# Optimization experiments

Measured on AMD Instinct MI355X. Metric: run time of the kernel, lower is better.

## Reference

```python
import jax, jax.numpy as jnp
import numpy as np

B, S, H, D = 4, 1024, 16, 64
DIM = H * D          # 1024
FF_INNER = 4 * DIM   # 4096
ROT_BASE = 1000.0


def _l2norm(x):
    # F.normalize(p=2, dim=-1): x / max(||x||_2, 1e-12)
    n = jnp.linalg.norm(x, axis=-1, keepdims=True)
    return x / jnp.maximum(n, 1e-12)


def _rmsnorm(x):
    return x * jax.lax.rsqrt(jnp.mean(x * x, axis=-1, keepdims=True) + jnp.finfo(jnp.float32).eps)


def _rope_tables(seq, d, base):
    inv_freq = base ** (-(jnp.arange(0, d, 2, dtype=jnp.float32) / d))
    freqs = jnp.outer(jnp.arange(seq, dtype=jnp.float32), inv_freq)  # [S, D/2]
    # original caches cos/sin in bfloat16
    cos = jnp.cos(freqs).astype(jnp.bfloat16)[None, :, None, :]
    sin = jnp.sin(freqs).astype(jnp.bfloat16)[None, :, None, :]
    return cos, sin


def _rope(x, cos, sin):
    d = x.shape[3] // 2
    x1, x2 = x[..., :d], x[..., d:]
    y1 = x1 * cos + x2 * sin
    y2 = -x1 * sin + x2 * cos
    return jnp.concatenate([y1, y2], axis=3).astype(x.dtype)


def setup_inputs() -> dict:
    key = jax.random.key(0)
    ks = jax.random.split(key, 12)
    w = lambda k, shp: 0.02 * jax.random.normal(k, shp, dtype=jnp.float32)
    inp = {
        'h_states': jax.random.normal(ks[0], (B, S, DIM), dtype=jnp.float32),
        'attention_mask': jnp.tril(jnp.ones((S, S), dtype=jnp.float32))[None].repeat(B, axis=0),
        'Wq': w(ks[1], (DIM, DIM)), 'Wk': w(ks[2], (DIM, DIM)), 'Wv': w(ks[3], (DIM, DIM)),
        'WqB': w(ks[4], (DIM, DIM)), 'WkB': w(ks[5], (DIM, DIM)),
        'Wo': w(ks[6], (DIM, DIM)), 'bo': jnp.zeros((DIM,), jnp.float32),
        'Wff_in': w(ks[7], (DIM, 2 * FF_INNER)), 'bff_in': jnp.zeros((2 * FF_INNER,), jnp.float32),
        'Wff_out': w(ks[8], (FF_INNER, DIM)), 'bff_out': jnp.zeros((DIM,), jnp.float32),
        'learnedlambda': jnp.asarray(1.0, jnp.float32),
        'l2normscale': jnp.log(jnp.asarray(float(S) ** 2 - float(S), jnp.float32)),
    }
    return inp


def reference(h_states, attention_mask, Wq, Wk, Wv, WqB, WkB, Wo, bo,
              Wff_in, bff_in, Wff_out, bff_out, learnedlambda, l2normscale):
    inner = _rmsnorm(h_states)                               # layerwisenorm (rmsnorm, no affine)
    scale = D ** -0.5

    def proj(Wm):
        return (inner @ Wm).reshape(B, S, H, D)
    q, k, v = proj(Wq), proj(Wk), proj(Wv)
    bq, bk = proj(WqB), proj(WkB)

    cos, sin = _rope_tables(S, D, ROT_BASE)
    q = _rope(_l2norm(q), cos, sin)
    k = _rope(_l2norm(k), cos, sin)
    bq = _rope(_l2norm(bq), cos, sin)
    bk = _rope(_l2norm(bk), cos, sin)

    # main branch: causal softmax attention, scale=1, scaled by learned l2normscale
    scores = jnp.einsum('bihd,bjhd->bhij', q, k)             # [B,H,S,S]
    causal = jnp.tril(jnp.ones((S, S), dtype=bool))
    scores = jnp.where(causal, scores, -jnp.inf)
    attn = jax.nn.softmax(scores, axis=-1)
    y = l2normscale * jnp.einsum('bhij,bjhd->bihd', attn, v)  # [B,S,H,D]

    # bias branch: softmax-free masked scores @ ones == row-sum broadcast over D
    bscores = jnp.einsum('bihd,bjhd->bhij', bq, bk) * scale
    bscores = bscores * attention_mask[:, None, :, :]
    brow = bscores.sum(axis=-1)                               # [B,H,S]
    y = y + jnp.transpose(brow, (0, 2, 1))[..., None]         # broadcast over D

    attn_out = y.reshape(B, S, DIM) @ Wo + bo

    # SwiGLU FFN: chunk -> x, gate; silu(gate) * x
    u = inner @ Wff_in + bff_in
    xh, gate = jnp.split(u, 2, axis=-1)
    dense_out = (jax.nn.silu(gate) * xh) @ Wff_out + bff_out

    return h_states * learnedlambda + dense_out + attn_out
```

## Files before the change

kernel.cpp:

```cpp
#include <hip/hip_runtime.h>
#include <stdint.h>
#include <math.h>

typedef float f32x4 __attribute__((ext_vector_type(4)));
typedef short s16x8 __attribute__((ext_vector_type(8)));
typedef unsigned short bfu;

#define AS1q const __attribute__((address_space(1))) void*
#define AS3q __attribute__((address_space(3))) void*

static __device__ __forceinline__ float bf2f(bfu v) {
  return __uint_as_float(((unsigned int)v) << 16);
}
static __device__ __forceinline__ bfu f2bf(float f) {
  unsigned int u = __float_as_uint(f);
  return (bfu)((u + 0x7fffu + ((u >> 16) & 1u)) >> 16);
}

struct PreArgs {
  const float* w5[5];
  const float* Wffin;
  const float* Wffout;
  const float* Wo;
  const float* h;
  bfu* wt5; bfu* wtfi; bfu* wtfoc;
  bfu* cosb; bfu* sinb; bfu* inner;
};
__global__ __launch_bounds__(256) void prologue_k(PreArgs a) {
  __shared__ float shmem[32 * 33];
  int id = blockIdx.x;
  if (id < 18432) {
    const float* W; bfu* Wt; int K, N, dstride, dofs, mode, nb, kb;
    if (id < 5120) {
      int z = id >> 10, rem = id & 1023;
      W = a.w5[z]; Wt = a.wt5 + ((size_t)z << 20);
      K = 1024; N = 1024; dstride = 1024; dofs = 0; mode = 0;
      nb = (rem & 31) << 5; kb = (rem >> 5) << 5;
    } else if (id < 13312) {
      int id2 = id - 5120;
      W = a.Wffin; Wt = a.wtfi; K = 1024; N = 8192; dstride = 1024; dofs = 0; mode = 1;
      nb = (id2 & 255) << 5; kb = (id2 >> 8) << 5;
    } else if (id < 17408) {
      int id3 = id - 13312;
      W = a.Wffout; Wt = a.wtfoc; K = 4096; N = 1024; dstride = 5120; dofs = 0; mode = 2;
      nb = (id3 & 31) << 5; kb = (id3 >> 5) << 5;
    } else {
      int id4 = id - 17408;
      W = a.Wo; Wt = a.wtfoc; K = 1024; N = 1024; dstride = 5120; dofs = 4096; mode = 2;
      nb = (id4 & 31) << 5; kb = (id4 >> 5) << 5;
    }
    float (*t)[33] = reinterpret_cast<float(*)[33]>(shmem);
    int tx = threadIdx.x & 31, ty = threadIdx.x >> 5;
#pragma unroll
    for (int i = 0; i < 4; i++) {
      int r = ty + i * 8;
      t[r][tx] = W[(size_t)(kb + r) * N + nb + tx];
    }
    __syncthreads();
#pragma unroll
    for (int i = 0; i < 4; i++) {
      int r = ty + i * 8;
      int n = nb + r;
      int nd = n;
      if (mode == 1) { int j = n & 4095, isg = n >> 12; nd = ((j >> 4) << 5) | (isg << 4) | (j & 15); }
      int k = kb + tx;
      int kp = (mode == 2) ? (((k >> 5) << 5) | ((k & 15) << 1) | ((k >> 4) & 1)) : k;
      Wt[(size_t)nd * dstride + dofs + kp] = f2bf(t[tx][r]);
    }
  } else if (id < 18560) {
    int idx = (id - 18432) * 256 + threadIdx.x;
    int s = idx >> 5, i = idx & 31;
    float f = powf(1000.0f, -(float)i / 32.0f);
    float fr = (float)s * f;
    a.cosb[idx] = f2bf(cosf(fr));
    a.sinb[idx] = f2bf(sinf(fr));
  } else {
    int row = id - 18560;
    const float* hr = a.h + (size_t)row * 1024;
    f32x4 x = *reinterpret_cast<const f32x4*>(hr + threadIdx.x * 4);
    float ss = x[0] * x[0] + x[1] * x[1] + x[2] * x[2] + x[3] * x[3];
    for (int off = 32; off; off >>= 1) ss += __shfl_down(ss, off);
    int wave = threadIdx.x >> 6, lane = threadIdx.x & 63;
    if (lane == 0) shmem[wave] = ss;
    __syncthreads();
    float tot = shmem[0] + shmem[1] + shmem[2] + shmem[3];
    float r = rsqrtf(tot * (1.0f / 1024.0f) + 1.1920929e-07f);
    bfu* o = a.inner + (size_t)row * 1024 + threadIdx.x * 4;
    o[0] = f2bf(x[0] * r); o[1] = f2bf(x[1] * r);
    o[2] = f2bf(x[2] * r); o[3] = f2bf(x[3] * r);
  }
}

__global__ __launch_bounds__(512, 2) void fused_k(const bfu* __restrict__ q, const bfu* __restrict__ k,
                                                  const bfu* __restrict__ vT,
                                                  const float* __restrict__ brow,
                                                  const float* __restrict__ l2p,
                                                  const bfu* __restrict__ A, const bfu* __restrict__ Bt,
                                                  bfu* __restrict__ AB,
                                                  const float* __restrict__ bias) {
  __shared__ __align__(16) char lds[131072];
  int tid = threadIdx.x, w = tid >> 6, lane = tid & 63;
  int g = lane >> 4, l15 = lane & 15;

  if (blockIdx.x < 256) {
    int fid = blockIdx.x + ((w >> 2) << 8);
    int sub = fid & 255;
    int qt = (fid >> 8) ? 7 - (sub >> 6) : (sub >> 6);
    int bh = sub & 63;
    const size_t bhofs = (size_t)bh << 16;
    int rt0 = qt * 128 + (w & 3) * 32;
    bfu* P = reinterpret_cast<bfu*>(lds) + (size_t)w * (2 * 16 * 72);

    s16x8 aq[2][2];
#pragma unroll
    for (int m = 0; m < 2; m++)
#pragma unroll
      for (int ks = 0; ks < 2; ks++)
        aq[m][ks] = *reinterpret_cast<const s16x8*>(
            q + bhofs + (size_t)(rt0 + m * 16 + l15) * 64 + ks * 32 + g * 8);

    f32x4 O[2][4];
    float mr[2][4], lr[2][4];
#pragma unroll
    for (int m = 0; m < 2; m++)
#pragma unroll
      for (int r = 0; r < 4; r++) { O[m][r] = (f32x4){0.f, 0.f, 0.f, 0.f}; mr[m][r] = -3.0e38f; lr[m][r] = 0.f; }

    s16x8 kA[4][2], kB[4][2];
    auto loadK = [&](s16x8 (&kd)[4][2], int jt) {
#pragma unroll
      for (int nt = 0; nt < 4; nt++)
#pragma unroll
        for (int ks = 0; ks < 2; ks++)
          kd[nt][ks] = *reinterpret_cast<const s16x8*>(
              k + bhofs + (size_t)(jt * 64 + nt * 16 + l15) * 64 + ks * 32 + g * 8);
    };

    int njt = 2 * qt + 2;
    loadK(kA, 0);

    auto body = [&](int jt, s16x8 (&kc)[4][2], s16x8 (&kn)[4][2], bool pf) {
      s16x8 vv[4][2];
#pragma unroll
      for (int nt = 0; nt < 4; nt++)
#pragma unroll
        for (int ks = 0; ks < 2; ks++)
          vv[nt][ks] = *reinterpret_cast<const s16x8*>(
              vT + ((size_t)(bh * 64 + nt * 16 + l15) << 10) + jt * 64 + ks * 32 + g * 8);

      bool act[2] = { jt * 64 <= rt0 + 15, jt * 64 <= rt0 + 31 };
      f32x4 sfr[2][4];
#pragma unroll
      for (int m = 0; m < 2; m++) {
        if (!act[m]) continue;
#pragma unroll
        for (int nt = 0; nt < 4; nt++) {
          sfr[m][nt] = (f32x4){0.f, 0.f, 0.f, 0.f};
#pragma unroll
          for (int ks = 0; ks < 2; ks++)
            sfr[m][nt] = __builtin_amdgcn_mfma_f32_16x16x32_bf16(aq[m][ks], kc[nt][ks], sfr[m][nt], 0, 0, 0);
        }
      }
      if (pf) loadK(kn, jt + 1);

#pragma unroll
      for (int m = 0; m < 2; m++) {
        if (!act[m]) continue;
        int rtm = rt0 + m * 16;
        if (jt * 64 + 63 > rtm) {
#pragma unroll
          for (int ntn = 0; ntn < 4; ntn++)
#pragma unroll
            for (int r = 0; r < 4; r++)
              if (jt * 64 + ntn * 16 + l15 > rtm + g * 4 + r) sfr[m][ntn][r] = -1e30f;
        }
        float alpha[4];
#pragma unroll
        for (int r = 0; r < 4; r++) {
          float v = fmaxf(fmaxf(sfr[m][0][r], sfr[m][1][r]), fmaxf(sfr[m][2][r], sfr[m][3][r]));
#pragma unroll
          for (int m2 = 1; m2 < 16; m2 <<= 1) v = fmaxf(v, __shfl_xor(v, m2));
          float mn = fmaxf(mr[m][r], v);
          alpha[r] = __expf(mr[m][r] - mn);
          mr[m][r] = mn;
        }
#pragma unroll
        for (int r = 0; r < 4; r++) {
          float rs = 0.f;
#pragma unroll
          for (int ntn = 0; ntn < 4; ntn++) {
            float e = __expf(sfr[m][ntn][r] - mr[m][r]);
            rs += e;
            P[(m * 16 + g * 4 + r) * 72 + ntn * 16 + l15] = f2bf(e);
          }
#pragma unroll
          for (int m2 = 1; m2 < 16; m2 <<= 1) rs += __shfl_xor(rs, m2);
          lr[m][r] = lr[m][r] * alpha[r] + rs;
#pragma unroll
          for (int ntn = 0; ntn < 4; ntn++) O[m][ntn][r] *= alpha[r];
        }
      }
      asm volatile("s_waitcnt lgkmcnt(0)" ::: "memory");
      __builtin_amdgcn_sched_barrier(0);
#pragma unroll
      for (int m = 0; m < 2; m++) {
        if (!act[m]) continue;
        s16x8 pa[2];
#pragma unroll
        for (int ks = 0; ks < 2; ks++)
          pa[ks] = *reinterpret_cast<const s16x8*>(&P[(m * 16 + l15) * 72 + ks * 32 + g * 8]);
#pragma unroll
        for (int nt = 0; nt < 4; nt++)
#pragma unroll
          for (int ks = 0; ks < 2; ks++)
            O[m][nt] = __builtin_amdgcn_mfma_f32_16x16x32_bf16(pa[ks], vv[nt][ks], O[m][nt], 0, 0, 0);
      }
    };

    for (int jt = 0; jt < njt; jt += 2) {
      body(jt, kA, kB, true);
      body(jt + 1, kB, kA, jt + 2 < njt);
    }

    float l2ns = l2p[0];
    int b = bh >> 4, hq = bh & 15;
#pragma unroll
    for (int m = 0; m < 2; m++)
#pragma unroll
      for (int r = 0; r < 4; r++) {
        int rowg = rt0 + m * 16 + g * 4 + r;
        float br = brow[bh * 1024 + rowg];
        float sc = l2ns / lr[m][r];
        float v0 = O[m][0][r] * sc + br;
        float v1 = O[m][1][r] * sc + br;
        float v2 = O[m][2][r] * sc + br;
        float v3 = O[m][3][r] * sc + br;
        unsigned int p01 = (unsigned int)f2bf(v0) | ((unsigned int)f2bf(v1) << 16);
        unsigned int p23 = (unsigned int)f2bf(v2) | ((unsigned int)f2bf(v3) << 16);
        size_t base = (size_t)(b * 1024 + rowg) * 5120 + 4096 + hq * 64;
        *reinterpret_cast<unsigned int*>(AB + base + 2 * l15) = p01;
        *reinterpret_cast<unsigned int*>(AB + base + 32 + 2 * l15) = p23;
      }
    return;
  }

  int id0 = blockIdx.x - 256;
  int c = id0 & 7, rr = id0 >> 3;
  int bn0 = (c & 3) * 8, bm0 = (c >> 2) * 8;
  int bm = bm0 + rr / 8, bn = bn0 + rr % 8;
  int wm = w >> 2, wn = w & 3;
  const int K = 1024;
  const int NT = 16, NI = 8;

  f32x4 acc[8][4];
#pragma unroll
  for (int m = 0; m < 8; m++)
#pragma unroll
    for (int n = 0; n < 4; n++) acc[m][n] = (f32x4){0.f, 0.f, 0.f, 0.f};

  s16x8 af[4][2];
  s16x8 bfr[4][2];

  auto stage = [&](int mat, int kt, int hf) {
    if (kt >= NT) return;
    int d = kt & 1;
    const bfu* s0 = (mat == 0) ? A : Bt;
    int rowbase = ((mat == 0) ? bm : bn) * 256 + hf * 128;
    int k0 = kt << 6;
    char* base = lds + d * 65536 + mat * 32768 + hf * 16384;
#pragma unroll
    for (int r = 0; r < 2; r++) {
      int L = r * 512 + tid;
      int row = L >> 3, cc = L & 7;
      int kc = cc ^ (row & 7);
      const bfu* src = s0 + (size_t)(rowbase + row) * K + k0 + kc * 8;
      char* dst = base + r * 8192 + w * 1024;
      __builtin_amdgcn_global_load_lds((AS1q)src, (AS3q)dst, 16, 0, 0);
    }
  };

  auto ldA = [&](int d, int mh) {
    const char* base = lds + d * 65536 + wm * 16384;
#pragma unroll
    for (int mm = 0; mm < 4; mm++) {
      int row = mh * 64 + mm * 16 + l15;
#pragma unroll
      for (int ks = 0; ks < 2; ks++)
        af[mm][ks] = *reinterpret_cast<const s16x8*>(
            base + row * 128 + (((ks * 4 + g) ^ (row & 7)) << 4));
    }
  };
  auto ldB2 = [&](int d, int nh) {
    const char* base = lds + d * 65536 + 32768 + (wn >> 1) * 16384;
#pragma unroll
    for (int nn = 0; nn < 2; nn++) {
      int row = (wn & 1) * 64 + (nh * 2 + nn) * 16 + l15;
#pragma unroll
      for (int ks = 0; ks < 2; ks++)
        bfr[nh * 2 + nn][ks] = *reinterpret_cast<const s16x8*>(
            base + row * 128 + (((ks * 4 + g) ^ (row & 7)) << 4));
    }
  };
  auto mfma_q = [&](int mh, int nh) {
    asm volatile("s_waitcnt lgkmcnt(0)" ::: "memory");
    __builtin_amdgcn_sched_barrier(0);
    __builtin_amdgcn_s_barrier();
    __builtin_amdgcn_s_setprio(1);
#pragma unroll
    for (int mm = 0; mm < 4; mm++)
#pragma unroll
      for (int nn = 0; nn < 2; nn++) {
        int n = nh * 2 + nn, m = mh * 4 + mm;
#pragma unroll
        for (int ks = 0; ks < 2; ks++)
          acc[m][n] = __builtin_amdgcn_mfma_f32_16x16x32_bf16(af[mm][ks], bfr[n][ks], acc[m][n], 0, 0, 0);
      }
    __builtin_amdgcn_s_setprio(0);
    __builtin_amdgcn_sched_barrier(0);
  };

  stage(1, 0, 0); stage(0, 0, 0); stage(0, 0, 1); stage(1, 0, 1);
  stage(1, 1, 0); stage(1, 1, 1);
  asm volatile("s_waitcnt vmcnt(4)" ::: "memory");
  __builtin_amdgcn_s_barrier();
  __builtin_amdgcn_sched_barrier(0);

  for (int i = 0; i < NI; i++) {
    int t0 = 2 * i, t1 = 2 * i + 1;
    bool last = (i == NI - 1);
    ldA(0, 0); ldB2(0, 0);
    stage(0, t1, 0);
    mfma_q(0, 0);
    ldB2(0, 1);
    stage(0, t1, 1);
    mfma_q(0, 1);
    ldA(0, 1);
    stage(1, t0 + 2, 0);
    mfma_q(1, 0);
    stage(1, t0 + 2, 1);
    mfma_q(1, 1);
    if (last) { asm volatile("s_waitcnt vmcnt(0)" ::: "memory"); }
    else      { asm volatile("s_waitcnt vmcnt(4)" ::: "memory"); }
    __builtin_amdgcn_s_barrier();
    __builtin_amdgcn_sched_barrier(0);
    ldA(1, 0); ldB2(1, 0);
    stage(0, t0 + 2, 0);
    mfma_q(0, 0);
    ldB2(1, 1);
    stage(0, t0 + 2, 1);
    mfma_q(0, 1);
    ldA(1, 1);
    stage(1, t1 + 2, 0);
    mfma_q(1, 0);
    stage(1, t1 + 2, 1);
    mfma_q(1, 1);
    asm volatile("s_waitcnt vmcnt(4)" ::: "memory");
    __builtin_amdgcn_s_barrier();
    __builtin_amdgcn_sched_barrier(0);
  }

  int j0 = (bn * 8 + wn * 2) * 16 + l15;
  float bx0 = bias[j0], bg0 = bias[j0 + 4096];
  float bx1 = bias[j0 + 16], bg1 = bias[j0 + 16 + 4096];
  int cb = (bn * 4 + wn) * 32 + 2 * l15;
#pragma unroll
  for (int m = 0; m < 8; m++) {
#pragma unroll
    for (int r = 0; r < 4; r++) {
      int row = bm * 256 + wm * 128 + m * 16 + g * 4 + r;
      float xh0 = acc[m][0][r] + bx0, gt0 = acc[m][1][r] + bg0;
      float xh1 = acc[m][2][r] + bx1, gt1 = acc[m][3][r] + bg1;
      float s0 = gt0 / (1.0f + __expf(-gt0)) * xh0;
      float s1 = gt1 / (1.0f + __expf(-gt1)) * xh1;
      unsigned int pk = (unsigned int)f2bf(s0) | ((unsigned int)f2bf(s1) << 16);
      *reinterpret_cast<unsigned int*>(AB + (size_t)row * 5120 + cb) = pk;
    }
  }
}

__global__ __launch_bounds__(256, 3) void gemm128p(const bfu* __restrict__ A, const bfu* __restrict__ Bt,
                                                   bfu* __restrict__ qb, bfu* __restrict__ kb,
                                                   bfu* __restrict__ vT,
                                                   bfu* __restrict__ bqh, bfu* __restrict__ bkh,
                                                   const bfu* __restrict__ ct, const bfu* __restrict__ st,
                                                   int M, int N, int K, int rbm, int rbn) {
  __shared__ __align__(16) char lds[49152];
  int nbx = N >> 7;
  int c = blockIdx.x & 7, rr = blockIdx.x >> 3;
  int ca = nbx / rbn;
  int bn0 = (c % ca) * rbn, bm0 = (c / ca) * rbm;
  int bm = bm0 + rr / rbn, bn = bn0 + rr % rbn;
  int tid = threadIdx.x, w = tid >> 6, lane = tid & 63;
  int wm = w >> 1, wn = w & 1;
  int g = lane >> 4, l15 = lane & 15;
  int NT = K >> 5;

  f32x4 acc[4][4];
#pragma unroll
  for (int m = 0; m < 4; m++)
#pragma unroll
    for (int n = 0; n < 4; n++) acc[m][n] = (f32x4){0.f, 0.f, 0.f, 0.f};

  auto stage = [&](int buf, int t) {
    int k0 = t << 5;
#pragma unroll
    for (int r = 0; r < 2; r++) {
      int L = r * 256 + tid;
      int row = L >> 2, cc = L & 3;
      int kc = cc ^ (row & 3);
      const bfu* srcA = A + (size_t)(bm * 128 + row) * K + k0 + kc * 8;
      char* dstA = lds + buf * 16384 + r * 4096 + w * 1024;
      __builtin_amdgcn_global_load_lds((AS1q)srcA, (AS3q)dstA, 16, 0, 0);
      const bfu* srcB = Bt + (size_t)(bn * 128 + row) * K + k0 + kc * 8;
      char* dstB = lds + buf * 16384 + 8192 + r * 4096 + w * 1024;
      __builtin_amdgcn_global_load_lds((AS1q)srcB, (AS3q)dstB, 16, 0, 0);
    }
  };

  stage(0, 0); stage(1, 1);
  asm volatile("s_waitcnt vmcnt(4)" ::: "memory");
  __builtin_amdgcn_s_barrier();
  __builtin_amdgcn_sched_barrier(0);

  int bc = 0;
  for (int t = 0; t < NT; t++) {
    int bs = bc + 2; if (bs >= 3) bs -= 3;
    if (t + 2 < NT) stage(bs, t + 2);
    const char* la = lds + bc * 16384;
    const char* lb = la + 8192;
    s16x8 af[4], bfr[4];
#pragma unroll
    for (int m = 0; m < 4; m++) {
      int row = wm * 64 + m * 16 + l15;
      af[m] = *reinterpret_cast<const s16x8*>(la + row * 64 + ((g ^ (row & 3)) << 4));
    }
#pragma unroll
    for (int n = 0; n < 4; n++) {
      int row = wn * 64 + n * 16 + l15;
      bfr[n] = *reinterpret_cast<const s16x8*>(lb + row * 64 + ((g ^ (row & 3)) << 4));
    }
    asm volatile("s_waitcnt lgkmcnt(0)" ::: "memory");
    __builtin_amdgcn_sched_barrier(0);
    __builtin_amdgcn_s_setprio(1);
#pragma unroll
    for (int m = 0; m < 4; m++)
#pragma unroll
      for (int n = 0; n < 4; n++)
        acc[m][n] = __builtin_amdgcn_mfma_f32_16x16x32_bf16(af[m], bfr[n], acc[m][n], 0, 0, 0);
// ... 14 lines not shown
    for (int m = 0; m < 4; m++) {
#pragma unroll
      for (int r = 0; r < 4; r++) {
        int sl = wm * 64 + m * 16 + g * 4 + r;
#pragma unroll
        for (int j = 0; j < 4; j++) {
          int d = j * 16 + l15;
          lv[(wn * 64 + d) * 136 + sl] = f2bf(acc[m][j][r]);
        }
      }
    }
    __syncthreads();
    int b = bm >> 3, h0 = (bn & 7) * 2;
#pragma unroll
    for (int i = 0; i < 8; i++) {
      int linear = i * 256 + tid;
      int hw = linear >> 10, rem = linear & 1023;
      int d = rem >> 4, sl8 = (rem & 15) << 3;
      s16x8 v8 = *reinterpret_cast<const s16x8*>(&lv[(hw * 64 + d) * 136 + sl8]);
      size_t dstofs = (((size_t)((b << 4) + h0 + hw) << 6) + d) * 1024 + (bm & 7) * 128 + sl8;
      *reinterpret_cast<s16x8*>(vT + dstofs) = v8;
    }
  } else {
#pragma unroll
    for (int m = 0; m < 4; m++) {
#pragma unroll
      for (int r = 0; r < 4; r++) {
        int row = bm * 128 + wm * 64 + m * 16 + g * 4 + r;
        int s = row & 1023, b = row >> 10;
        float a0 = acc[m][0][r], a1 = acc[m][1][r];
        float a2 = acc[m][2][r], a3 = acc[m][3][r];
        float ss = a0 * a0 + a1 * a1 + a2 * a2 + a3 * a3;
        ss += __shfl_xor(ss, 1); ss += __shfl_xor(ss, 2);
        ss += __shfl_xor(ss, 4); ss += __shfl_xor(ss, 8);
        float inv = 1.0f / fmaxf(sqrtf(ss), 1e-12f);
        float xn0 = a0 * inv, xn1 = a1 * inv, xn2 = a2 * inv, xn3 = a3 * inv;
        float c0 = bf2f(ct[(s << 5) + l15]),      s0v = bf2f(st[(s << 5) + l15]);
        float c1 = bf2f(ct[(s << 5) + 16 + l15]), s1v = bf2f(st[(s << 5) + 16 + l15]);
        float o0 = xn0 * c0 + xn2 * s0v;
        float o1 = xn1 * c1 + xn3 * s1v;
        float o2 = xn2 * c0 - xn0 * s0v;
        float o3 = xn3 * c1 - xn1 * s1v;
        unsigned long long pk =
            (unsigned long long)((unsigned int)f2bf(o0) | ((unsigned int)f2bf(o1) << 16)) |
            ((unsigned long long)((unsigned int)f2bf(o2) | ((unsigned int)f2bf(o3) << 16)) << 32);
        size_t base = ((((size_t)((b << 4) + hh) << 10) + s) << 6) + (l15 << 2);
        bfu* dst = (which == 0) ? qb : (which == 1) ? kb : (which == 3) ? bqh : bkh;
        *reinterpret_cast<unsigned long long*>(dst + base) = pk;
      }
    }
  }
}

__global__ __launch_bounds__(256, 3) void gemm128f(const bfu* __restrict__ A, const bfu* __restrict__ Bt,
                                                   float* __restrict__ out,
                                                   const float* __restrict__ b1,
                                                   const float* __restrict__ b2,
                                                   const float* __restrict__ lam,
                                                   const float* __restrict__ h,
                                                   int M, int N, int K, int rbm, int rbn) {
  __shared__ __align__(16) char lds[98304];
  int nbx = N >> 7;
  int c = blockIdx.x & 7, rr = blockIdx.x >> 3;
  int ca = nbx / rbn;
  int bn0 = (c % ca) * rbn, bm0 = (c / ca) * rbm;
  int bm = bm0 + rr / rbn, bn = bn0 + rr % rbn;
  int tid = threadIdx.x, w = tid >> 6, lane = tid & 63;
  int wm = w >> 1, wn = w & 1;
  int g = lane >> 4, l15 = lane & 15;
  int NT = K >> 6;

  f32x4 acc[4][4];
#pragma unroll
  for (int m = 0; m < 4; m++)
#pragma unroll
    for (int n = 0; n < 4; n++) acc[m][n] = (f32x4){0.f, 0.f, 0.f, 0.f};

  auto stage = [&](int buf, int t) {
    int k0 = t << 6;
#pragma unroll
    for (int r = 0; r < 4; r++) {
      int L = r * 256 + tid;
      int row = L >> 3, cc = L & 7;
      int kc = cc ^ (row & 7);
      const bfu* srcA = A + (size_t)(bm * 128 + row) * K + k0 + kc * 8;
      char* dstA = lds + buf * 32768 + r * 4096 + w * 1024;
      __builtin_amdgcn_global_load_lds((AS1q)srcA, (AS3q)dstA, 16, 0, 0);
    }
#pragma unroll
    for (int r = 0; r < 4; r++) {
      int L = r * 256 + tid;
      int row = L >> 3, cc = L & 7;
      int kc = cc ^ (row & 7);
      const bfu* srcB = Bt + (size_t)(bn * 128 + row) * K + k0 + kc * 8;
      char* dstB = lds + buf * 32768 + 16384 + r * 4096 + w * 1024;
      __builtin_amdgcn_global_load_lds((AS1q)srcB, (AS3q)dstB, 16, 0, 0);
    }
  };

  stage(0, 0); stage(1, 1);
  asm volatile("s_waitcnt vmcnt(8)" ::: "memory");
  __builtin_amdgcn_s_barrier();
  __builtin_amdgcn_sched_barrier(0);

  int bc = 0;
  for (int t = 0; t < NT; t++) {
// ... 63 lines not shown
  float s = 0.f;
  for (int j = 0; j < 128; j++) s += bf2f(bk[base + (size_t)j * 64]);
  csums[wave][lane] = s;
  __syncthreads();
  float p = 0.f;
  for (int cc = 0; cc < wave; cc++) p += csums[cc][lane];
  for (int j = 0; j < 128; j++) {
    p += bf2f(bk[base + (size_t)j * 64]);
    float t = bf2f(bq[base + (size_t)j * 64]) * p;
#pragma unroll
    for (int m2 = 1; m2 < 64; m2 <<= 1) t += __shfl_xor(t, m2);
    if (lane == 0) brow[bh * 1024 + wave * 128 + j] = 0.125f * t;
  }
}

extern "C" void kernel_launch(void* const* d_in, const int* in_sizes, int n_in,
                              void* d_out, int out_size, void* d_ws, size_t ws_size,
                              hipStream_t stream) {
  const float* h      = (const float*)d_in[0];
  const float* Wq     = (const float*)d_in[2];
  const float* Wk     = (const float*)d_in[3];
  const float* Wv     = (const float*)d_in[4];
  const float* WqB    = (const float*)d_in[5];
  const float* WkB    = (const float*)d_in[6];
  const float* Wo     = (const float*)d_in[7];
  const float* bo     = (const float*)d_in[8];
  const float* Wffin  = (const float*)d_in[9];
  const float* bffin  = (const float*)d_in[10];
  const float* Wffout = (const float*)d_in[11];
  const float* bffout = (const float*)d_in[12];
  const float* lam    = (const float*)d_in[13];
  const float* l2ns   = (const float*)d_in[14];
  float* out = (float*)d_out;

  char* ws = (char*)d_ws;
  size_t off = 0;
  auto alloc = [&](size_t bytes) { void* p = ws + off; off += bytes; return p; };
  bfu* wt5   = (bfu*)alloc(5ull * 1024 * 1024 * 2);
  bfu* wtfi  = (bfu*)alloc(8192ull * 1024 * 2);
  bfu* wtfoc = (bfu*)alloc(1024ull * 5120 * 2);
  bfu* cosb  = (bfu*)alloc(1024ull * 32 * 2);
  bfu* sinb  = (bfu*)alloc(1024ull * 32 * 2);
  bfu* inner = (bfu*)alloc(4096ull * 1024 * 2);
  bfu* qb    = (bfu*)alloc(64ull * 1024 * 64 * 2);
  bfu* kb    = (bfu*)alloc(64ull * 1024 * 64 * 2);
  bfu* vtb   = (bfu*)alloc(64ull * 1024 * 64 * 2);
  bfu* bqh   = (bfu*)alloc(64ull * 1024 * 64 * 2);
  bfu* bkh   = (bfu*)alloc(64ull * 1024 * 64 * 2);
  float* browb = (float*)alloc(64ull * 1024 * 4);
  bfu* AB    = (bfu*)alloc(4096ull * 5120 * 2);

  PreArgs pa;
  pa.w5[0] = Wq; pa.w5[1] = Wk; pa.w5[2] = Wv; pa.w5[3] = WqB; pa.w5[4] = WkB;
  pa.Wffin = Wffin; pa.Wffout = Wffout; pa.Wo = Wo; pa.h = h;
  pa.wt5 = wt5; pa.wtfi = wtfi; pa.wtfoc = wtfoc;
  pa.cosb = cosb; pa.sinb = sinb; pa.inner = inner;
  prologue_k<<<dim3(22656), 256, 0, stream>>>(pa);

  gemm128p<<<dim3(1280), 256, 0, stream>>>(inner, wt5, qb, kb, vtb, bqh, bkh, cosb, sinb,
                                           4096, 5120, 1024, 32, 5);

  brow_all<<<dim3(64), 512, 0, stream>>>(bqh, bkh, browb);

  fused_k<<<dim3(768), 512, 0, stream>>>(qb, kb, vtb, browb, l2ns,
                                         inner, wtfi, AB, bffin);

  gemm128f<<<dim3(256), 256, 0, stream>>>(AB, wtfoc, out, bffout, bo, lam, h,
                                          4096, 1024, 5120, 8, 4);
}
```

Measured before the change: 304.6 us.

## Move FFN/Wo weight conversion into projection GEMM launch to overlap

The FFN-in, FFN-out and Wo weight transpose/bf16 conversions move out of the prologue and into extra blocks appended to the QKV projection GEMM kernel. The prologue then only converts the five projection weights, the rope tables and the rmsnorm, so the projection GEMM can start sooner while the remaining conversions run alongside its tail. The projection GEMM's block mapping is hardcoded for its fixed shape. The extra 13312 conversion blocks share the 256-thread, 48KB-LDS launch configuration, which may limit how many conversion blocks fit per CU.

Result: no change. 299.3 us, median of 2 (-1.7%).

```diff
diff --git a/kernel.cpp b/kernel.cpp
--- a/kernel.cpp
+++ b/kernel.cpp
@@ -19,63 +19,40 @@
 
 struct PreArgs {
   const float* w5[5];
-  const float* Wffin;
-  const float* Wffout;
-  const float* Wo;
   const float* h;
-  bfu* wt5; bfu* wtfi; bfu* wtfoc;
+  bfu* wt5;
   bfu* cosb; bfu* sinb; bfu* inner;
 };
 __global__ __launch_bounds__(256) void prologue_k(PreArgs a) {
   __shared__ float shmem[32 * 33];
   int id = blockIdx.x;
-  if (id < 18432) {
-    const float* W; bfu* Wt; int K, N, dstride, dofs, mode, nb, kb;
-    if (id < 5120) {
-      int z = id >> 10, rem = id & 1023;
-      W = a.w5[z]; Wt = a.wt5 + ((size_t)z << 20);
-      K = 1024; N = 1024; dstride = 1024; dofs = 0; mode = 0;
-      nb = (rem & 31) << 5; kb = (rem >> 5) << 5;
-    } else if (id < 13312) {
-      int id2 = id - 5120;
-      W = a.Wffin; Wt = a.wtfi; K = 1024; N = 8192; dstride = 1024; dofs = 0; mode = 1;
-      nb = (id2 & 255) << 5; kb = (id2 >> 8) << 5;
-    } else if (id < 17408) {
-      int id3 = id - 13312;
-      W = a.Wffout; Wt = a.wtfoc; K = 4096; N = 1024; dstride = 5120; dofs = 0; mode = 2;
-      nb = (id3 & 31) << 5; kb = (id3 >> 5) << 5;
-    } else {
-      int id4 = id - 17408;
-      W = a.Wo; Wt = a.wtfoc; K = 1024; N = 1024; dstride = 5120; dofs = 4096; mode = 2;
-      nb = (id4 & 31) << 5; kb = (id4 >> 5) << 5;
-    }
+  if (id < 5120) {
+    int z = id >> 10, rem = id & 1023;
+    const float* W = a.w5[z];
+    bfu* Wt = a.wt5 + ((size_t)z << 20);
+    int nb = (rem & 31) << 5, kb = (rem >> 5) << 5;
     float (*t)[33] = reinterpret_cast<float(*)[33]>(shmem);
     int tx = threadIdx.x & 31, ty = threadIdx.x >> 5;
 #pragma unroll
     for (int i = 0; i < 4; i++) {
       int r = ty + i * 8;
-      t[r][tx] = W[(size_t)(kb + r) * N + nb + tx];
+      t[r][tx] = W[(size_t)(kb + r) * 1024 + nb + tx];
     }
     __syncthreads();
 #pragma unroll
     for (int i = 0; i < 4; i++) {
       int r = ty + i * 8;
-      int n = nb + r;
-      int nd = n;
-      if (mode == 1) { int j = n & 4095, isg = n >> 12; nd = ((j >> 4) << 5) | (isg << 4) | (j & 15); }
-      int k = kb + tx;
-      int kp = (mode == 2) ? (((k >> 5) << 5) | ((k & 15) << 1) | ((k >> 4) & 1)) : k;
-      Wt[(size_t)nd * dstride + dofs + kp] = f2bf(t[tx][r]);
-    }
-  } else if (id < 18560) {
-    int idx = (id - 18432) * 256 + threadIdx.x;
+      Wt[(size_t)(nb + r) * 1024 + kb + tx] = f2bf(t[tx][r]);
+    }
+  } else if (id < 5248) {
+    int idx = (id - 5120) * 256 + threadIdx.x;
     int s = idx >> 5, i = idx & 31;
     float f = powf(1000.0f, -(float)i / 32.0f);
     float fr = (float)s * f;
     a.cosb[idx] = f2bf(cosf(fr));
     a.sinb[idx] = f2bf(sinf(fr));
   } else {
-    int row = id - 18560;
+    int row = id - 5248;
     const float* hr = a.h + (size_t)row * 1024;
     f32x4 x = *reinterpret_cast<const f32x4*>(hr + threadIdx.x * 4);
     float ss = x[0] * x[0] + x[1] * x[1] + x[2] * x[2] + x[3] * x[3];
@@ -91,309 +68,61 @@
   }
 }
 
-__global__ __launch_bounds__(512, 2) void fused_k(const bfu* __restrict__ q, const bfu* __restrict__ k,
-                                                  const bfu* __restrict__ vT,
-                                                  const float* __restrict__ brow,
-                                                  const float* __restrict__ l2p,
-                                                  const bfu* __restrict__ A, const bfu* __restrict__ Bt,
-                                                  bfu* __restrict__ AB,
-                                                  const float* __restrict__ bias) {
-  __shared__ __align__(16) char lds[131072];
+__global__ __launch_bounds__(256, 3) void projconv_k(const bfu* __restrict__ A, const bfu* __restrict__ Bt,
+                                                     bfu* __restrict__ qb, bfu* __restrict__ kb,
+                                                     bfu* __restrict__ vT,
+                                                     bfu* __restrict__ bqh, bfu* __restrict__ bkh,
+                                                     const bfu* __restrict__ ct, const bfu* __restrict__ st,
+                                                     const float* __restrict__ Wffin,
+                                                     const float* __restrict__ Wffout,
+                                                     const float* __restrict__ Wo,
+                                                     bfu* __restrict__ wtfi, bfu* __restrict__ wtfoc) {
+  __shared__ __align__(16) char lds[49152];
   int tid = threadIdx.x, w = tid >> 6, lane = tid & 63;
   int g = lane >> 4, l15 = lane & 15;
 
-  if (blockIdx.x < 256) {
-    int fid = blockIdx.x + ((w >> 2) << 8);
-    int sub = fid & 255;
-    int qt = (fid >> 8) ? 7 - (sub >> 6) : (sub >> 6);
-    int bh = sub & 63;
-    const size_t bhofs = (size_t)bh << 16;
-    int rt0 = qt * 128 + (w & 3) * 32;
-    bfu* P = reinterpret_cast<bfu*>(lds) + (size_t)w * (2 * 16 * 72);
-
-    s16x8 aq[2][2];
-#pragma unroll
-    for (int m = 0; m < 2; m++)
-#pragma unroll
-      for (int ks = 0; ks < 2; ks++)
-        aq[m][ks] = *reinterpret_cast<const s16x8*>(
-            q + bhofs + (size_t)(rt0 + m * 16 + l15) * 64 + ks * 32 + g * 8);
-
-    f32x4 O[2][4];
-    float mr[2][4], lr[2][4];
-#pragma unroll
-    for (int m = 0; m < 2; m++)
-#pragma unroll
-      for (int r = 0; r < 4; r++) { O[m][r] = (f32x4){0.f, 0.f, 0.f, 0.f}; mr[m][r] = -3.0e38f; lr[m][r] = 0.f; }
-
-    s16x8 kA[4][2], kB[4][2];
-    auto loadK = [&](s16x8 (&kd)[4][2], int jt) {
-#pragma unroll
-      for (int nt = 0; nt < 4; nt++)
-#pragma unroll
-        for (int ks = 0; ks < 2; ks++)
-          kd[nt][ks] = *reinterpret_cast<const s16x8*>(
-              k + bhofs + (size_t)(jt * 64 + nt * 16 + l15) * 64 + ks * 32 + g * 8);
-    };
-
-    int njt = 2 * qt + 2;
-    loadK(kA, 0);
-
-    auto body = [&](int jt, s16x8 (&kc)[4][2], s16x8 (&kn)[4][2], bool pf) {
-      s16x8 vv[4][2];
-#pragma unroll
-      for (int nt = 0; nt < 4; nt++)
-#pragma unroll
-        for (int ks = 0; ks < 2; ks++)
-          vv[nt][ks] = *reinterpret_cast<const s16x8*>(
-              vT + ((size_t)(bh * 64 + nt * 16 + l15) << 10) + jt * 64 + ks * 32 + g * 8);
-
-      bool act[2] = { jt * 64 <= rt0 + 15, jt * 64 <= rt0 + 31 };
-      f32x4 sfr[2][4];
-#pragma unroll
-      for (int m = 0; m < 2; m++) {
-        if (!act[m]) continue;
-#pragma unroll
-        for (int nt = 0; nt < 4; nt++) {
-          sfr[m][nt] = (f32x4){0.f, 0.f, 0.f, 0.f};
-#pragma unroll
-          for (int ks = 0; ks < 2; ks++)
-            sfr[m][nt] = __builtin_amdgcn_mfma_f32_16x16x32_bf16(aq[m][ks], kc[nt][ks], sfr[m][nt], 0, 0, 0);
-        }
-      }
-      if (pf) loadK(kn, jt + 1);
-
-#pragma unroll
-      for (int m = 0; m < 2; m++) {
-        if (!act[m]) continue;
-        int rtm = rt0 + m * 16;
-        if (jt * 64 + 63 > rtm) {
-#pragma unroll
-          for (int ntn = 0; ntn < 4; ntn++)
-#pragma unroll
-            for (int r = 0; r < 4; r++)
-              if (jt * 64 + ntn * 16 + l15 > rtm + g * 4 + r) sfr[m][ntn][r] = -1e30f;
-        }
-        float alpha[4];
-#pragma unroll
-        for (int r = 0; r < 4; r++) {
-          float v = fmaxf(fmaxf(sfr[m][0][r], sfr[m][1][r]), fmaxf(sfr[m][2][r], sfr[m][3][r]));
-#pragma unroll
-          for (int m2 = 1; m2 < 16; m2 <<= 1) v = fmaxf(v, __shfl_xor(v, m2));
-          float mn = fmaxf(mr[m][r], v);
-          alpha[r] = __expf(mr[m][r] - mn);
-          mr[m][r] = mn;
-        }
-#pragma unroll
-        for (int r = 0; r < 4; r++) {
-          float rs = 0.f;
-#pragma unroll
-          for (int ntn = 0; ntn < 4; ntn++) {
-            float e = __expf(sfr[m][ntn][r] - mr[m][r]);
-            rs += e;
-            P[(m * 16 + g * 4 + r) * 72 + ntn * 16 + l15] = f2bf(e);
-          }
-#pragma unroll
-          for (int m2 = 1; m2 < 16; m2 <<= 1) rs += __shfl_xor(rs, m2);
-          lr[m][r] = lr[m][r] * alpha[r] + rs;
-#pragma unroll
-          for (int ntn = 0; ntn < 4; ntn++) O[m][ntn][r] *= alpha[r];
-        }
-      }
-      asm volatile("s_waitcnt lgkmcnt(0)" ::: "memory");
-      __builtin_amdgcn_sched_barrier(0);
-#pragma unroll
-      for (int m = 0; m < 2; m++) {
-        if (!act[m]) continue;
-        s16x8 pa[2];
-#pragma unroll
-        for (int ks = 0; ks < 2; ks++)
-          pa[ks] = *reinterpret_cast<const s16x8*>(&P[(m * 16 + l15) * 72 + ks * 32 + g * 8]);
-#pragma unroll
-        for (int nt = 0; nt < 4; nt++)
-#pragma unroll
-          for (int ks = 0; ks < 2; ks++)
-            O[m][nt] = __builtin_amdgcn_mfma_f32_16x16x32_bf16(pa[ks], vv[nt][ks], O[m][nt], 0, 0, 0);
-      }
-    };
-
-    for (int jt = 0; jt < njt; jt += 2) {
-      body(jt, kA, kB, true);
-      body(jt + 1, kB, kA, jt + 2 < njt);
-    }
-
-    float l2ns = l2p[0];
-    int b = bh >> 4, hq = bh & 15;
-#pragma unroll
-    for (int m = 0; m < 2; m++)
-#pragma unroll
-      for (int r = 0; r < 4; r++) {
-        int rowg = rt0 + m * 16 + g * 4 + r;
-        float br = brow[bh * 1024 + rowg];
-        float sc = l2ns / lr[m][r];
-        float v0 = O[m][0][r] * sc + br;
-        float v1 = O[m][1][r] * sc + br;
-        float v2 = O[m][2][r] * sc + br;
-        float v3 = O[m][3][r] * sc + br;
-        unsigned int p01 = (unsigned int)f2bf(v0) | ((unsigned int)f2bf(v1) << 16);
-        unsigned int p23 = (unsigned int)f2bf(v2) | ((unsigned int)f2bf(v3) << 16);
-        size_t base = (size_t)(b * 1024 + rowg) * 5120 + 4096 + hq * 64;
-        *reinterpret_cast<unsigned int*>(AB + base + 2 * l15) = p01;
-        *reinterpret_cast<unsigned int*>(AB + base + 32 + 2 * l15) = p23;
-      }
+  if (blockIdx.x >= 1280) {
+    int cid = blockIdx.x - 1280;
+    const float* W; bfu* Wt; int N, dstride, dofs, mode, nb, kb2;
+    if (cid < 8192) {
+      W = Wffin; Wt = wtfi; N = 8192; dstride = 1024; dofs = 0; mode = 1;
+      nb = (cid & 255) << 5; kb2 = (cid >> 8) << 5;
+    } else if (cid < 12288) {
+      int id3 = cid - 8192;
+      W = Wffout; Wt = wtfoc; N = 1024; dstride = 5120; dofs = 0; mode = 2;
+      nb = (id3 & 31) << 5; kb2 = (id3 >> 5) << 5;
+    } else {
+      int id4 = cid - 12288;
+      W = Wo; Wt = wtfoc; N = 1024; dstride = 5120; dofs = 4096; mode = 2;
+      nb = (id4 & 31) << 5; kb2 = (id4 >> 5) << 5;
+    }
+    float (*t)[33] = reinterpret_cast<float(*)[33]>(lds);
+    int tx = tid & 31, ty = tid >> 5;
+#pragma unroll
+    for (int i = 0; i < 4; i++) {
+      int r = ty + i * 8;
+      t[r][tx] = W[(size_t)(kb2 + r) * N + nb + tx];
+    }
+    __syncthreads();
+#pragma unroll
+    for (int i = 0; i < 4; i++) {
+      int r = ty + i * 8;
+      int n = nb + r;
+      int nd = n;
+      if (mode == 1) { int j = n & 4095, isg = n >> 12; nd = ((j >> 4) << 5) | (isg << 4) | (j & 15); }
+      int k = kb2 + tx;
+      int kp = (mode == 2) ? (((k >> 5) << 5) | ((k & 15) << 1) | ((k >> 4) & 1)) : k;
+      Wt[(size_t)nd * dstride + dofs + kp] = f2bf(t[tx][r]);
+    }
     return;
   }
 
-  int id0 = blockIdx.x - 256;
-  int c = id0 & 7, rr = id0 >> 3;
-  int bn0 = (c & 3) * 8, bm0 = (c >> 2) * 8;
-  int bm = bm0 + rr / 8, bn = bn0 + rr % 8;
-  int wm = w >> 2, wn = w & 3;
   const int K = 1024;
-  const int NT = 16, NI = 8;
-
-  f32x4 acc[8][4];
-#pragma unroll
-  for (int m = 0; m < 8; m++)
-#pragma unroll
-    for (int n = 0; n < 4; n++) acc[m][n] = (f32x4){0.f, 0.f, 0.f, 0.f};
-
-  s16x8 af[4][2];
-  s16x8 bfr[4][2];
-
-  auto stage = [&](int mat, int kt, int hf) {
-    if (kt >= NT) return;
-    int d = kt & 1;
-    const bfu* s0 = (mat == 0) ? A : Bt;
-    int rowbase = ((mat == 0) ? bm : bn) * 256 + hf * 128;
-    int k0 = kt << 6;
-    char* base = lds + d * 65536 + mat * 32768 + hf * 16384;
-#pragma unroll
-    for (int r = 0; r < 2; r++) {
-      int L = r * 512 + tid;
-      int row = L >> 3, cc = L & 7;
-      int kc = cc ^ (row & 7);
-      const bfu* src = s0 + (size_t)(rowbase + row) * K + k0 + kc * 8;
-      char* dst = base + r * 8192 + w * 1024;
-      __builtin_amdgcn_global_load_lds((AS1q)src, (AS3q)dst, 16, 0, 0);
-    }
-  };
-
-  auto ldA = [&](int d, int mh) {
-    const char* base = lds + d * 65536 + wm * 16384;
-#pragma unroll
-    for (int mm = 0; mm < 4; mm++) {
-      int row = mh * 64 + mm * 16 + l15;
-#pragma unroll
-      for (int ks = 0; ks < 2; ks++)
-        af[mm][ks] = *reinterpret_cast<const s16x8*>(
-            base + row * 128 + (((ks * 4 + g) ^ (row & 7)) << 4));
-    }
-  };
-  auto ldB2 = [&](int d, int nh) {
-    const char* base = lds + d * 65536 + 32768 + (wn >> 1) * 16384;
-#pragma unroll
-    for (int nn = 0; nn < 2; nn++) {
-      int row = (wn & 1) * 64 + (nh * 2 + nn) * 16 + l15;
-#pragma unroll
-      for (int ks = 0; ks < 2; ks++)
-        bfr[nh * 2 + nn][ks] = *reinterpret_cast<const s16x8*>(
-            base + row * 128 + (((ks * 4 + g) ^ (row & 7)) << 4));
-    }
-  };
-  auto mfma_q = [&](int mh, int nh) {
-    asm volatile("s_waitcnt lgkmcnt(0)" ::: "memory");
-    __builtin_amdgcn_sched_barrier(0);
-    __builtin_amdgcn_s_barrier();
-    __builtin_amdgcn_s_setprio(1);
-#pragma unroll
-    for (int mm = 0; mm < 4; mm++)
-#pragma unroll
-      for (int nn = 0; nn < 2; nn++) {
-        int n = nh * 2 + nn, m = mh * 4 + mm;
-#pragma unroll
-        for (int ks = 0; ks < 2; ks++)
-          acc[m][n] = __builtin_amdgcn_mfma_f32_16x16x32_bf16(af[mm][ks], bfr[n][ks], acc[m][n], 0, 0, 0);
-      }
-    __builtin_amdgcn_s_setprio(0);
-    __builtin_amdgcn_sched_barrier(0);
-  };
-
-  stage(1, 0, 0); stage(0, 0, 0); stage(0, 0, 1); stage(1, 0, 1);
-  stage(1, 1, 0); stage(1, 1, 1);
-  asm volatile("s_waitcnt vmcnt(4)" ::: "memory");
-  __builtin_amdgcn_s_barrier();
-  __builtin_amdgcn_sched_barrier(0);
-
-  for (int i = 0; i < NI; i++) {
-    int t0 = 2 * i, t1 = 2 * i + 1;
-    bool last = (i == NI - 1);
-    ldA(0, 0); ldB2(0, 0);
-    stage(0, t1, 0);
-    mfma_q(0, 0);
-    ldB2(0, 1);
-    stage(0, t1, 1);
-    mfma_q(0, 1);
-    ldA(0, 1);
-    stage(1, t0 + 2, 0);
-    mfma_q(1, 0);
-    stage(1, t0 + 2, 1);
-    mfma_q(1, 1);
-    if (last) { asm volatile("s_waitcnt vmcnt(0)" ::: "memory"); }
-    else      { asm volatile("s_waitcnt vmcnt(4)" ::: "memory"); }
-    __builtin_amdgcn_s_barrier();
-    __builtin_amdgcn_sched_barrier(0);
-    ldA(1, 0); ldB2(1, 0);
-    stage(0, t0 + 2, 0);
-    mfma_q(0, 0);
-    ldB2(1, 1);
-    stage(0, t0 + 2, 1);
-    mfma_q(0, 1);
-    ldA(1, 1);
-    stage(1, t1 + 2, 0);
-    mfma_q(1, 0);
-    stage(1, t1 + 2, 1);
-    mfma_q(1, 1);
-    asm volatile("s_waitcnt vmcnt(4)" ::: "memory");
-    __builtin_amdgcn_s_barrier();
-    __builtin_amdgcn_sched_barrier(0);
-  }
-
-  int j0 = (bn * 8 + wn * 2) * 16 + l15;
-  float bx0 = bias[j0], bg0 = bias[j0 + 4096];
-  float bx1 = bias[j0 + 16], bg1 = bias[j0 + 16 + 4096];
-  int cb = (bn * 4 + wn) * 32 + 2 * l15;
-#pragma unroll
-  for (int m = 0; m < 8; m++) {
-#pragma unroll
-    for (int r = 0; r < 4; r++) {
-      int row = bm * 256 + wm * 128 + m * 16 + g * 4 + r;
-      float xh0 = acc[m][0][r] + bx0, gt0 = acc[m][1][r] + bg0;
-      float xh1 = acc[m][2][r] + bx1, gt1 = acc[m][3][r] + bg1;
-      float s0 = gt0 / (1.0f + __expf(-gt0)) * xh0;
-      float s1 = gt1 / (1.0f + __expf(-gt1)) * xh1;
-      unsigned int pk = (unsigned int)f2bf(s0) | ((unsigned int)f2bf(s1) << 16);
-      *reinterpret_cast<unsigned int*>(AB + (size_t)row * 5120 + cb) = pk;
-    }
-  }
-}
-
-__global__ __launch_bounds__(256, 3) void gemm128p(const bfu* __restrict__ A, const bfu* __restrict__ Bt,
-                                                   bfu* __restrict__ qb, bfu* __restrict__ kb,
-                                                   bfu* __restrict__ vT,
-                                                   bfu* __restrict__ bqh, bfu* __restrict__ bkh,
-                                                   const bfu* __restrict__ ct, const bfu* __restrict__ st,
-                                                   int M, int N, int K, int rbm, int rbn) {
-  __shared__ __align__(16) char lds[49152];
-  int nbx = N >> 7;
   int c = blockIdx.x & 7, rr = blockIdx.x >> 3;
-  int ca = nbx / rbn;
-  int bn0 = (c % ca) * rbn, bm0 = (c / ca) * rbm;
-  int bm = bm0 + rr / rbn, bn = bn0 + rr % rbn;
-  int tid = threadIdx.x, w = tid >> 6, lane = tid & 63;
+  int bn0 = c * 5;
+  int bm = rr / 5, bn = bn0 + rr % 5;
   int wm = w >> 1, wn = w & 1;
-  int g = lane >> 4, l15 = lane & 15;
-  int NT = K >> 5;
+  const int NT = 32;
 
   f32x4 acc[4][4];
 #pragma unroll
@@ -514,6 +243,293 @@
   }
 }
 
+__global__ __launch_bounds__(512, 2) void fused_k(const bfu* __restrict__ q, const bfu* __restrict__ k,
+                                                  const bfu* __restrict__ vT,
+                                                  const float* __restrict__ brow,
+                                                  const float* __restrict__ l2p,
+                                                  const bfu* __restrict__ A, const bfu* __restrict__ Bt,
+                                                  bfu* __restrict__ AB,
+                                                  const float* __restrict__ bias) {
+  __shared__ __align__(16) char lds[131072];
+  int tid = threadIdx.x, w = tid >> 6, lane = tid & 63;
+  int g = lane >> 4, l15 = lane & 15;
+
+  if (blockIdx.x < 256) {
+    int fid = blockIdx.x + ((w >> 2) << 8);
+    int sub = fid & 255;
+    int qt = (fid >> 8) ? 7 - (sub >> 6) : (sub >> 6);
+    int bh = sub & 63;
+    const size_t bhofs = (size_t)bh << 16;
+    int rt0 = qt * 128 + (w & 3) * 32;
+    bfu* P = reinterpret_cast<bfu*>(lds) + (size_t)w * (2 * 16 * 72);
+
+    s16x8 aq[2][2];
+#pragma unroll
+    for (int m = 0; m < 2; m++)
+#pragma unroll
+      for (int ks = 0; ks < 2; ks++)
+        aq[m][ks] = *reinterpret_cast<const s16x8*>(
+            q + bhofs + (size_t)(rt0 + m * 16 + l15) * 64 + ks * 32 + g * 8);
+
+    f32x4 O[2][4];
+    float mr[2][4], lr[2][4];
+#pragma unroll
+    for (int m = 0; m < 2; m++)
+#pragma unroll
+      for (int r = 0; r < 4; r++) { O[m][r] = (f32x4){0.f, 0.f, 0.f, 0.f}; mr[m][r] = -3.0e38f; lr[m][r] = 0.f; }
+
+    s16x8 kA[4][2], kB[4][2];
+    auto loadK = [&](s16x8 (&kd)[4][2], int jt) {
+#pragma unroll
+      for (int nt = 0; nt < 4; nt++)
+#pragma unroll
+        for (int ks = 0; ks < 2; ks++)
+          kd[nt][ks] = *reinterpret_cast<const s16x8*>(
+              k + bhofs + (size_t)(jt * 64 + nt * 16 + l15) * 64 + ks * 32 + g * 8);
+    };
+
+    int njt = 2 * qt + 2;
+    loadK(kA, 0);
+
+    auto body = [&](int jt, s16x8 (&kc)[4][2], s16x8 (&kn)[4][2], bool pf) {
+      s16x8 vv[4][2];
+#pragma unroll
+      for (int nt = 0; nt < 4; nt++)
+#pragma unroll
+        for (int ks = 0; ks < 2; ks++)
+          vv[nt][ks] = *reinterpret_cast<const s16x8*>(
+              vT + ((size_t)(bh * 64 + nt * 16 + l15) << 10) + jt * 64 + ks * 32 + g * 8);
+
+      bool act[2] = { jt * 64 <= rt0 + 15, jt * 64 <= rt0 + 31 };
+      f32x4 sfr[2][4];
+#pragma unroll
+      for (int m = 0; m < 2; m++) {
+        if (!act[m]) continue;
+#pragma unroll
+        for (int nt = 0; nt < 4; nt++) {
+          sfr[m][nt] = (f32x4){0.f, 0.f, 0.f, 0.f};
+#pragma unroll
+          for (int ks = 0; ks < 2; ks++)
+            sfr[m][nt] = __builtin_amdgcn_mfma_f32_16x16x32_bf16(aq[m][ks], kc[nt][ks], sfr[m][nt], 0, 0, 0);
+        }
+      }
+      if (pf) loadK(kn, jt + 1);
+
+#pragma unroll
+      for (int m = 0; m < 2; m++) {
+        if (!act[m]) continue;
+        int rtm = rt0 + m * 16;
+        if (jt * 64 + 63 > rtm) {
+#pragma unroll
+          for (int ntn = 0; ntn < 4; ntn++)
+#pragma unroll
+            for (int r = 0; r < 4; r++)
+              if (jt * 64 + ntn * 16 + l15 > rtm + g * 4 + r) sfr[m][ntn][r] = -1e30f;
+        }
+        float alpha[4];
+#pragma unroll
+        for (int r = 0; r < 4; r++) {
+          float v = fmaxf(fmaxf(sfr[m][0][r], sfr[m][1][r]), fmaxf(sfr[m][2][r], sfr[m][3][r]));
+#pragma unroll
+          for (int m2 = 1; m2 < 16; m2 <<= 1) v = fmaxf(v, __shfl_xor(v, m2));
+          float mn = fmaxf(mr[m][r], v);
+          alpha[r] = __expf(mr[m][r] - mn);
+          mr[m][r] = mn;
+        }
+#pragma unroll
+        for (int r = 0; r < 4; r++) {
+          float rs = 0.f;
+#pragma unroll
+          for (int ntn = 0; ntn < 4; ntn++) {
+            float e = __expf(sfr[m][ntn][r] - mr[m][r]);
+            rs += e;
+            P[(m * 16 + g * 4 + r) * 72 + ntn * 16 + l15] = f2bf(e);
+          }
+#pragma unroll
+          for (int m2 = 1; m2 < 16; m2 <<= 1) rs += __shfl_xor(rs, m2);
+          lr[m][r] = lr[m][r] * alpha[r] + rs;
+#pragma unroll
+          for (int ntn = 0; ntn < 4; ntn++) O[m][ntn][r] *= alpha[r];
+        }
+      }
+      asm volatile("s_waitcnt lgkmcnt(0)" ::: "memory");
+      __builtin_amdgcn_sched_barrier(0);
+#pragma unroll
+      for (int m = 0; m < 2; m++) {
+        if (!act[m]) continue;
+        s16x8 pa[2];
+#pragma unroll
+        for (int ks = 0; ks < 2; ks++)
+          pa[ks] = *reinterpret_cast<const s16x8*>(&P[(m * 16 + l15) * 72 + ks * 32 + g * 8]);
+#pragma unroll
+        for (int nt = 0; nt < 4; nt++)
+#pragma unroll
+          for (int ks = 0; ks < 2; ks++)
+            O[m][nt] = __builtin_amdgcn_mfma_f32_16x16x32_bf16(pa[ks], vv[nt][ks], O[m][nt], 0, 0, 0);
+      }
+    };
+
+    for (int jt = 0; jt < njt; jt += 2) {
+      body(jt, kA, kB, true);
+      body(jt + 1, kB, kA, jt + 2 < njt);
+    }
+
+    float l2ns = l2p[0];
+    int b = bh >> 4, hq = bh & 15;
+#pragma unroll
+    for (int m = 0; m < 2; m++)
+#pragma unroll
+      for (int r = 0; r < 4; r++) {
+        int rowg = rt0 + m * 16 + g * 4 + r;
+        float br = brow[bh * 1024 + rowg];
+        float sc = l2ns / lr[m][r];
+        float v0 = O[m][0][r] * sc + br;
+        float v1 = O[m][1][r] * sc + br;
+        float v2 = O[m][2][r] * sc + br;
+        float v3 = O[m][3][r] * sc + br;
+        unsigned int p01 = (unsigned int)f2bf(v0) | ((unsigned int)f2bf(v1) << 16);
+        unsigned int p23 = (unsigned int)f2bf(v2) | ((unsigned int)f2bf(v3) << 16);
+        size_t base = (size_t)(b * 1024 + rowg) * 5120 + 4096 + hq * 64;
+        *reinterpret_cast<unsigned int*>(AB + base + 2 * l15) = p01;
+        *reinterpret_cast<unsigned int*>(AB + base + 32 + 2 * l15) = p23;
+      }
+    return;
+  }
+
+  int id0 = blockIdx.x - 256;
+  int c = id0 & 7, rr = id0 >> 3;
+  int bn0 = (c & 3) * 8, bm0 = (c >> 2) * 8;
+  int bm = bm0 + rr / 8, bn = bn0 + rr % 8;
+  int wm = w >> 2, wn = w & 3;
+  const int K = 1024;
+  const int NT = 16, NI = 8;
+
+  f32x4 acc[8][4];
+#pragma unroll
+  for (int m = 0; m < 8; m++)
+#pragma unroll
+    for (int n = 0; n < 4; n++) acc[m][n] = (f32x4){0.f, 0.f, 0.f, 0.f};
+
+  s16x8 af[4][2];
+  s16x8 bfr[4][2];
+
+  auto stage = [&](int mat, int kt, int hf) {
+    if (kt >= NT) return;
+    int d = kt & 1;
+    const bfu* s0 = (mat == 0) ? A : Bt;
+    int rowbase = ((mat == 0) ? bm : bn) * 256 + hf * 128;
+    int k0 = kt << 6;
+    char* base = lds + d * 65536 + mat * 32768 + hf * 16384;
+#pragma unroll
+    for (int r = 0; r < 2; r++) {
+      int L = r * 512 + tid;
+      int row = L >> 3, cc = L & 7;
+      int kc = cc ^ (row & 7);
+      const bfu* src = s0 + (size_t)(rowbase + row) * K + k0 + kc * 8;
+      char* dst = base + r * 8192 + w * 1024;
+      __builtin_amdgcn_global_load_lds((AS1q)src, (AS3q)dst, 16, 0, 0);
+    }
+  };
+
+  auto ldA = [&](int d, int mh) {
+    const char* base = lds + d * 65536 + wm * 16384;
+#pragma unroll
+    for (int mm = 0; mm < 4; mm++) {
+      int row = mh * 64 + mm * 16 + l15;
+#pragma unroll
+      for (int ks = 0; ks < 2; ks++)
+        af[mm][ks] = *reinterpret_cast<const s16x8*>(
+            base + row * 128 + (((ks * 4 + g) ^ (row & 7)) << 4));
+    }
+  };
+  auto ldB2 = [&](int d, int nh) {
+    const char* base = lds + d * 65536 + 32768 + (wn >> 1) * 16384;
+#pragma unroll
+    for (int nn = 0; nn < 2; nn++) {
+      int row = (wn & 1) * 64 + (nh * 2 + nn) * 16 + l15;
+#pragma unroll
+      for (int ks = 0; ks < 2; ks++)
+        bfr[nh * 2 + nn][ks] = *reinterpret_cast<const s16x8*>(
+            base + row * 128 + (((ks * 4 + g) ^ (row & 7)) << 4));
+    }
+  };
+  auto mfma_q = [&](int mh, int nh) {
+    asm volatile("s_waitcnt lgkmcnt(0)" ::: "memory");
+    __builtin_amdgcn_sched_barrier(0);
+    __builtin_amdgcn_s_barrier();
+    __builtin_amdgcn_s_setprio(1);
+#pragma unroll
+    for (int mm = 0; mm < 4; mm++)
+#pragma unroll
+      for (int nn = 0; nn < 2; nn++) {
+        int n = nh * 2 + nn, m = mh * 4 + mm;
+#pragma unroll
+        for (int ks = 0; ks < 2; ks++)
+          acc[m][n] = __builtin_amdgcn_mfma_f32_16x16x32_bf16(af[mm][ks], bfr[n][ks], acc[m][n], 0, 0, 0);
+      }
+    __builtin_amdgcn_s_setprio(0);
+    __builtin_amdgcn_sched_barrier(0);
+  };
+
+  stage(1, 0, 0); stage(0, 0, 0); stage(0, 0, 1); stage(1, 0, 1);
+  stage(1, 1, 0); stage(1, 1, 1);
+  asm volatile("s_waitcnt vmcnt(4)" ::: "memory");
+  __builtin_amdgcn_s_barrier();
+  __builtin_amdgcn_sched_barrier(0);
+
+  for (int i = 0; i < NI; i++) {
+    int t0 = 2 * i, t1 = 2 * i + 1;
+    bool last = (i == NI - 1);
+    ldA(0, 0); ldB2(0, 0);
+    stage(0, t1, 0);
+    mfma_q(0, 0);
+    ldB2(0, 1);
+    stage(0, t1, 1);
+    mfma_q(0, 1);
+    ldA(0, 1);
+    stage(1, t0 + 2, 0);
+    mfma_q(1, 0);
+    stage(1, t0 + 2, 1);
+    mfma_q(1, 1);
+    if (last) { asm volatile("s_waitcnt vmcnt(0)" ::: "memory"); }
+    else      { asm volatile("s_waitcnt vmcnt(4)" ::: "memory"); }
+    __builtin_amdgcn_s_barrier();
+    __builtin_amdgcn_sched_barrier(0);
+    ldA(1, 0); ldB2(1, 0);
+    stage(0, t0 + 2, 0);
+    mfma_q(0, 0);
+    ldB2(1, 1);
+    stage(0, t0 + 2, 1);
+    mfma_q(0, 1);
+    ldA(1, 1);
+    stage(1, t1 + 2, 0);
+    mfma_q(1, 0);
+    stage(1, t1 + 2, 1);
+    mfma_q(1, 1);
+    asm volatile("s_waitcnt vmcnt(4)" ::: "memory");
+    __builtin_amdgcn_s_barrier();
+    __builtin_amdgcn_sched_barrier(0);
+  }
+
+  int j0 = (bn * 8 + wn * 2) * 16 + l15;
+  float bx0 = bias[j0], bg0 = bias[j0 + 4096];
+  float bx1 = bias[j0 + 16], bg1 = bias[j0 + 16 + 4096];
+  int cb = (bn * 4 + wn) * 32 + 2 * l15;
+#pragma unroll
+  for (int m = 0; m < 8; m++) {
+#pragma unroll
+    for (int r = 0; r < 4; r++) {
+      int row = bm * 256 + wm * 128 + m * 16 + g * 4 + r;
+      float xh0 = acc[m][0][r] + bx0, gt0 = acc[m][1][r] + bg0;
+      float xh1 = acc[m][2][r] + bx1, gt1 = acc[m][3][r] + bg1;
+      float s0 = gt0 / (1.0f + __expf(-gt0)) * xh0;
+      float s1 = gt1 / (1.0f + __expf(-gt1)) * xh1;
+      unsigned int pk = (unsigned int)f2bf(s0) | ((unsigned int)f2bf(s1) << 16);
+      *reinterpret_cast<unsigned int*>(AB + (size_t)row * 5120 + cb) = pk;
+    }
+  }
+}
+
 __global__ __launch_bounds__(256, 3) void gemm128f(const bfu* __restrict__ A, const bfu* __restrict__ Bt,
                                                    float* __restrict__ out,
                                                    const float* __restrict__ b1,
@@ -683,13 +699,11 @@
 
   PreArgs pa;
   pa.w5[0] = Wq; pa.w5[1] = Wk; pa.w5[2] = Wv; pa.w5[3] = WqB; pa.w5[4] = WkB;
-  pa.Wffin = Wffin; pa.Wffout = Wffout; pa.Wo = Wo; pa.h = h;
-  pa.wt5 = wt5; pa.wtfi = wtfi; pa.wtfoc = wtfoc;
-  pa.cosb = cosb; pa.sinb = sinb; pa.inner = inner;
-  prologue_k<<<dim3(22656), 256, 0, stream>>>(pa);
-
-  gemm128p<<<dim3(1280), 256, 0, stream>>>(inner, wt5, qb, kb, vtb, bqh, bkh, cosb, sinb,
-                                           4096, 5120, 1024, 32, 5);
+  pa.h = h; pa.wt5 = wt5; pa.cosb = cosb; pa.sinb = sinb; pa.inner = inner;
+  prologue_k<<<dim3(9344), 256, 0, stream>>>(pa);
+
+  projconv_k<<<dim3(14592), 256, 0, stream>>>(inner, wt5, qb, kb, vtb, bqh, bkh, cosb, sinb,
+                                              Wffin, Wffout, Wo, wtfi, wtfoc);
 
   brow_all<<<dim3(64), 512, 0, stream>>>(bqh, bkh, browb);
 
```
